# Optimization experiments

Measured on AMD Instinct MI355X. Metric: run time of the kernel, lower is better.

Reference implementation:

```python
import jax, jax.numpy as jnp
import numpy as np

N_NODES = 50000
N_EDGES = 1600000
N_GRAPHS = 64
IN_DIM = 128
HID = 128
N_CLASSES = 10


def setup_inputs() -> dict:
    key = jax.random.key(0)
    ks = jax.random.split(key, 12)
    x = jax.random.normal(ks[0], (N_NODES, IN_DIM), dtype=jnp.float32)
    edge_index = jax.random.randint(ks[1], (2, N_EDGES), 0, N_NODES, dtype=jnp.int32)
    batch = jnp.sort(jax.random.randint(ks[2], (N_NODES,), 0, N_GRAPHS, dtype=jnp.int32))
    def glorot(k, shape):
        s = 1.0 / np.sqrt(shape[0])
        return jax.random.uniform(k, shape, jnp.float32, -s, s)
    W1 = glorot(ks[3], (IN_DIM, HID)); b1 = jnp.zeros((HID,), jnp.float32)
    W2 = glorot(ks[4], (HID, HID));    b2 = jnp.zeros((HID,), jnp.float32)
    Wc1 = glorot(ks[5], (HID, HID));   bc1 = glorot(ks[6], (HID,))
    Wc2 = glorot(ks[7], (HID, N_CLASSES)); bc2 = glorot(ks[8], (N_CLASSES,))
    return {"x": x, "edge_index": edge_index, "batch": batch,
            "W1": W1, "b1": b1, "W2": W2, "b2": b2,
            "Wc1": Wc1, "bc1": bc1, "Wc2": Wc2, "bc2": bc2}


def gcn_conv(x, edge_index, W, b):
    """PyG GCNConv: sym-normalized A-hat (with self loops) @ (x W) + b."""
    n = x.shape[0]
    loop = jnp.arange(n, dtype=edge_index.dtype)
    src = jnp.concatenate([edge_index[0], loop])  # message source
    dst = jnp.concatenate([edge_index[1], loop])  # message target
    deg = jax.ops.segment_sum(jnp.ones_like(src, dtype=x.dtype), dst, num_segments=n)
    dinv = jnp.where(deg > 0, jax.lax.rsqrt(deg), jnp.zeros_like(deg))
    norm = dinv[src] * dinv[dst]  # [E+N]
    h = x @ W                     # [N, H]
    msg = h[src] * norm[:, None]  # gather + scale
    out = jax.ops.segment_sum(msg, dst, num_segments=n)
    return out + b


def reference(x, edge_index, batch, W1, b1, W2, b2, Wc1, bc1, Wc2, bc2):
    h = jax.nn.relu(gcn_conv(x, edge_index, W1, b1))
    h = jax.nn.relu(gcn_conv(h, edge_index, W2, b2))
    # per-graph mean pooling (segment mean)
    sums = jax.ops.segment_sum(h, batch, num_segments=N_GRAPHS)
    cnt = jax.ops.segment_sum(jnp.ones((h.shape[0],), h.dtype), batch, num_segments=N_GRAPHS)
    g = sums / jnp.clip(cnt, 1.0)[:, None]  # [G, H]
    z = jax.nn.relu(g @ Wc1 + bc1)
    return z @ Wc2 + bc2
```

## Files before the change

kernel.cpp:

```cpp
#include <hip/hip_runtime.h>
#include <cstdint>
#include <cstddef>

#define CHUNK 4096

typedef __attribute__((ext_vector_type(8))) short short8;
typedef __attribute__((ext_vector_type(4))) float f32x4;
typedef __attribute__((ext_vector_type(4))) unsigned int u32x4;

__device__ __forceinline__ float bf2f(unsigned short u) {
  return __uint_as_float(((unsigned)u) << 16);
}
__device__ __forceinline__ unsigned short f2bf(float f) {
  unsigned u = __float_as_uint(f);
  u += 0x7fffu + ((u >> 16) & 1u);
  return (unsigned short)(u >> 16);
}

union SMem {
  unsigned short ws[128 * 136];
  struct { int c[256]; int cur[256]; int sb[256]; } cf;
};

__global__ void prep_k(const float* __restrict__ W1, const float* __restrict__ W2,
                       unsigned short* __restrict__ W1t, unsigned short* __restrict__ W2t,
                       int* __restrict__ gcur, int B) {
  int idx = blockIdx.x * 256 + threadIdx.x;
  const float* W = (idx < 16384) ? W1 : W2;
  unsigned short* Wt = (idx < 16384) ? W1t : W2t;
  int i = idx & 16383;
  int k = i >> 7, n = i & 127;
  Wt[n * 128 + k] = f2bf(W[i]);
  if (blockIdx.x == 0 && threadIdx.x < B) gcur[threadIdx.x] = 0;
}

__global__ __launch_bounds__(256) void scatter_atomic_k(const int* __restrict__ src,
                                                        const int* __restrict__ dst, int E,
                                                        int* __restrict__ gcur,
                                                        unsigned int* __restrict__ tmp,
                                                        int cap, int B) {
  __shared__ unsigned pk[CHUNK];
  __shared__ unsigned char bk[CHUNK];
  __shared__ int h[256];
  __shared__ int cur[256];
  __shared__ int base_s[256];
  int t = threadIdx.x;
  h[t] = 0;
  __syncthreads();
  int e0 = blockIdx.x * CHUNK;
  int e1 = e0 + CHUNK; if (e1 > E) e1 = E;
  int m = e1 - e0;
  for (int i = t; i < m; i += 256) {
    int d = dst[e0 + i], s = src[e0 + i];
    int b = d >> 8;
    pk[i] = ((unsigned)s << 8) | (unsigned)(d & 255);
    bk[i] = (unsigned char)b;
    atomicAdd(&h[b], 1);
  }
  __syncthreads();
  if (t < B && h[t] > 0) base_s[t] = atomicAdd(&gcur[t], h[t]);
  cur[t] = 0;
  __syncthreads();
  for (int i = t; i < m; i += 256) {
    int b = bk[i];
    int r = atomicAdd(&cur[b], 1);
    int p = base_s[b] + r;
    if (p < cap) tmp[(size_t)b * cap + p] = pk[i];
  }
}

template <bool AF32>
__device__ __forceinline__ void gemm_tile(SMem& sm, const void* Ap,
                                          const unsigned short* Wt,
                                          unsigned short* C, int N, int tile) {
  for (int idx = threadIdx.x; idx < 2048; idx += 256) {
    int n = idx >> 4, c = idx & 15;
    *(uint4*)&sm.ws[n * 136 + c * 8] = ((const uint4*)Wt)[idx];
  }
  __syncthreads();
  const int w = threadIdx.x >> 6;
  const int lane = threadIdx.x & 63;
  const int quad = lane >> 4, l16 = lane & 15;
  const int rb = tile * 128 + w * 32;
  f32x4 acc[2][8] = {};
  #pragma unroll
  for (int ks = 0; ks < 4; ks++) {
    short8 aF[2];
    #pragma unroll
    for (int m = 0; m < 2; m++) {
      int r = rb + m * 16 + l16;
      short8 a = {};
      if (r < N) {
        if (AF32) {
          const float* ar = (const float*)Ap + (size_t)r * 128 + ks * 32 + quad * 8;
          float4 u0 = *(const float4*)ar;
          float4 u1 = *(const float4*)(ar + 4);
          a[0] = (short)f2bf(u0.x); a[1] = (short)f2bf(u0.y);
          a[2] = (short)f2bf(u0.z); a[3] = (short)f2bf(u0.w);
          a[4] = (short)f2bf(u1.x); a[5] = (short)f2bf(u1.y);
          a[6] = (short)f2bf(u1.z); a[7] = (short)f2bf(u1.w);
        } else {
          a = *(const short8*)((const unsigned short*)Ap + (size_t)r * 128 + ks * 32 + quad * 8);
        }
      }
      aF[m] = a;
    }
    #pragma unroll
    for (int t = 0; t < 8; t++) {
      short8 bF = *(const short8*)&sm.ws[(t * 16 + l16) * 136 + ks * 32 + quad * 8];
      acc[0][t] = __builtin_amdgcn_mfma_f32_16x16x32_bf16(aF[0], bF, acc[0][t], 0, 0, 0);
      acc[1][t] = __builtin_amdgcn_mfma_f32_16x16x32_bf16(aF[1], bF, acc[1][t], 0, 0, 0);
    }
  }
  __syncthreads();
  unsigned short* Cs = sm.ws;
  #pragma unroll
  for (int m = 0; m < 2; m++) {
    int rloc = w * 32 + m * 16 + quad * 4;
    #pragma unroll
    for (int t = 0; t < 8; t++)
      #pragma unroll
      for (int rg = 0; rg < 4; rg++)
        Cs[(rloc + rg) * 132 + t * 16 + l16] = f2bf(acc[m][t][rg]);
  }
  __syncthreads();
  const int r0 = tile * 128;
  for (int idx = threadIdx.x; idx < 2048; idx += 256) {
    int row = idx >> 4, c = idx & 15;
    int rr = r0 + row;
    if (rr < N) {
      uint2 a = *(uint2*)&Cs[row * 132 + c * 8];
      uint2 b = *(uint2*)&Cs[row * 132 + c * 8 + 4];
      ((uint4*)C)[(size_t)rr * 16 + c] = make_uint4(a.x, a.y, b.x, b.y);
    }
  }
}

__global__ __launch_bounds__(256) void cntfill_gemm1_k(const unsigned int* __restrict__ tmp,
                                                       const int* __restrict__ gcur,
                                                       int N, int E, int cap, int B,
                                                       float* __restrict__ dinv,
                                                       int* __restrict__ rs,
                                                       unsigned short* __restrict__ col,
                                                       const float* __restrict__ x,
                                                       const unsigned short* __restrict__ W1t,
                                                       unsigned short* __restrict__ B2) {
  __shared__ SMem sm;
  const int t = threadIdx.x;
  if ((int)blockIdx.x >= B) {
    gemm_tile<true>(sm, x, W1t, B2, N, blockIdx.x - B);
    return;
  }
  int b = blockIdx.x;
  int cb = 0;
  if (t < B) { cb = gcur[t]; if (cb > cap) cb = cap; }
  sm.cf.sb[t] = cb;
  __syncthreads();
  for (int off = 1; off < 256; off <<= 1) {
    int u = (t >= off) ? sm.cf.sb[t - off] : 0;
    __syncthreads();
    sm.cf.sb[t] += u;
    __syncthreads();
  }
  int base_b = (b > 0) ? sm.cf.sb[b - 1] : 0;
  int cnt_b = sm.cf.sb[b] - base_b;
  if (b == 0 && t == 0) rs[N] = sm.cf.sb[B - 1];
  const unsigned* tb = tmp + (size_t)b * cap;
  sm.cf.c[t] = 0;
  __syncthreads();
  for (int i = t; i < cnt_b; i += 256) atomicAdd(&sm.cf.c[tb[i] & 255u], 1);
  __syncthreads();
  int v = sm.cf.c[t];
  sm.cf.cur[t] = v;
  __syncthreads();
  for (int off = 1; off < 256; off <<= 1) {
    int u = (t >= off) ? sm.cf.cur[t - off] : 0;
    __syncthreads();
    sm.cf.cur[t] += u;
    __syncthreads();
  }
  int rsv = base_b + sm.cf.cur[t] - v;
  int node = (b << 8) + t;
  if (node < N) {
    rs[node] = rsv;
    dinv[node] = rsqrtf((float)v + 1.0f);
  }
  __syncthreads();
  sm.cf.cur[t] = rsv;
  __syncthreads();
  for (int i = t; i < cnt_b; i += 256) {
    unsigned u = tb[i];
    int pos = atomicAdd(&sm.cf.cur[u & 255u], 1);
    col[pos] = (unsigned short)(u >> 8);
  }
}

template <bool AF32>
__global__ __launch_bounds__(256) void gemm_bf_k(const void* __restrict__ Ap,
                                                 const unsigned short* __restrict__ Wt,
                                                 unsigned short* __restrict__ C, int N) {
  __shared__ SMem sm;
  gemm_tile<AF32>(sm, Ap, Wt, C, N, blockIdx.x);
}

template <typename CT>
__global__ __launch_bounds__(256) void agg16_k(const unsigned short* __restrict__ h,
                                               const int* __restrict__ rs,
                                               const CT* __restrict__ col,
                                               const float* __restrict__ dinv,
                                               const float* __restrict__ bias,
                                               unsigned short* __restrict__ outp, int n) {
  int wid = (blockIdx.x * blockDim.x + threadIdx.x) >> 6;
  int lane = threadIdx.x & 63;
  if (wid >= n) return;
  const int g = lane >> 4;
  const int l = lane & 15;
  float di = dinv[wid];
  float acc[8];
  {
    uint4 sv = ((const uint4*)(h + (size_t)wid * 128))[l];
    float ws = (g == 0) ? di : 0.f;
    acc[0] = bf2f((unsigned short)sv.x) * ws;
    acc[1] = bf2f((unsigned short)(sv.x >> 16)) * ws;
    acc[2] = bf2f((unsigned short)sv.y) * ws;
    acc[3] = bf2f((unsigned short)(sv.y >> 16)) * ws;
    acc[4] = bf2f((unsigned short)sv.z) * ws;
    acc[5] = bf2f((unsigned short)(sv.z >> 16)) * ws;
    acc[6] = bf2f((unsigned short)sv.w) * ws;
    acc[7] = bf2f((unsigned short)(sv.w >> 16)) * ws;
  }
  int beg = rs[wid], end = rs[wid + 1];
  for (int base = beg; base < end; base += 16) {
    int e0 = base + g, e1 = base + 4 + g, e2 = base + 8 + g, e3 = base + 12 + g;
    int i0 = (e0 < end) ? e0 : end - 1;
    int i1 = (e1 < end) ? e1 : end - 1;
    int i2 = (e2 < end) ? e2 : end - 1;
    int i3 = (e3 < end) ? e3 : end - 1;
    int s0 = (int)col[i0], s1 = (int)col[i1], s2 = (int)col[i2], s3 = (int)col[i3];
    float w0 = (e0 < end) ? dinv[s0] : 0.f;
    float w1 = (e1 < end) ? dinv[s1] : 0.f;
    float w2 = (e2 < end) ? dinv[s2] : 0.f;
    float w3 = (e3 < end) ? dinv[s3] : 0.f;
    uint4 h0 = ((const uint4*)(h + (size_t)s0 * 128))[l];
    uint4 h1 = ((const uint4*)(h + (size_t)s1 * 128))[l];
    uint4 h2 = ((const uint4*)(h + (size_t)s2 * 128))[l];
    uint4 h3 = ((const uint4*)(h + (size_t)s3 * 128))[l];
    acc[0] += bf2f((unsigned short)h0.x) * w0 + bf2f((unsigned short)h1.x) * w1
            + bf2f((unsigned short)h2.x) * w2 + bf2f((unsigned short)h3.x) * w3;
    acc[1] += bf2f((unsigned short)(h0.x >> 16)) * w0 + bf2f((unsigned short)(h1.x >> 16)) * w1
            + bf2f((unsigned short)(h2.x >> 16)) * w2 + bf2f((unsigned short)(h3.x >> 16)) * w3;
    acc[2] += bf2f((unsigned short)h0.y) * w0 + bf2f((unsigned short)h1.y) * w1
            + bf2f((unsigned short)h2.y) * w2 + bf2f((unsigned short)h3.y) * w3;
    acc[3] += bf2f((unsigned short)(h0.y >> 16)) * w0 + bf2f((unsigned short)(h1.y >> 16)) * w1
            + bf2f((unsigned short)(h2.y >> 16)) * w2 + bf2f((unsigned short)(h3.y >> 16)) * w3;
    acc[4] += bf2f((unsigned short)h0.z) * w0 + bf2f((unsigned short)h1.z) * w1
            + bf2f((unsigned short)h2.z) * w2 + bf2f((unsigned short)h3.z) * w3;
    acc[5] += bf2f((unsigned short)(h0.z >> 16)) * w0 + bf2f((unsigned short)(h1.z >> 16)) * w1
            + bf2f((unsigned short)(h2.z >> 16)) * w2 + bf2f((unsigned short)(h3.z >> 16)) * w3;
    acc[6] += bf2f((unsigned short)h0.w) * w0 + bf2f((unsigned short)h1.w) * w1
            + bf2f((unsigned short)h2.w) * w2 + bf2f((unsigned short)h3.w) * w3;
    acc[7] += bf2f((unsigned short)(h0.w >> 16)) * w0 + bf2f((unsigned short)(h1.w >> 16)) * w1
            + bf2f((unsigned short)(h2.w >> 16)) * w2 + bf2f((unsigned short)(h3.w >> 16)) * w3;
  }
  #pragma unroll
  for (int j = 0; j < 8; j++) {
    acc[j] += __shfl_xor(acc[j], 16);
    acc[j] += __shfl_xor(acc[j], 32);
  }
  if (g == 0) {
    float4 bA = *(const float4*)(bias + l * 8);
    float4 bB = *(const float4*)(bias + l * 8 + 4);
    float r0 = fmaxf(acc[0] * di + bA.x, 0.f);
    float r1 = fmaxf(acc[1] * di + bA.y, 0.f);
    float r2 = fmaxf(acc[2] * di + bA.z, 0.f);
    float r3 = fmaxf(acc[3] * di + bA.w, 0.f);
    float r4 = fmaxf(acc[4] * di + bB.x, 0.f);
    float r5 = fmaxf(acc[5] * di + bB.y, 0.f);
    float r6 = fmaxf(acc[6] * di + bB.z, 0.f);
    float r7 = fmaxf(acc[7] * di + bB.w, 0.f);
    u32x4 v;
    v.x = (unsigned)f2bf(r0) | ((unsigned)f2bf(r1) << 16);
    v.y = (unsigned)f2bf(r2) | ((unsigned)f2bf(r3) << 16);
    v.z = (unsigned)f2bf(r4) | ((unsigned)f2bf(r5) << 16);
    v.w = (unsigned)f2bf(r6) | ((unsigned)f2bf(r7) << 16);
    __builtin_nontemporal_store(v, (u32x4*)outp + (size_t)wid * 16 + l);
  }
}

__global__ __launch_bounds__(256) void poolclassify2_k(const unsigned short* __restrict__ h,
                                                       const int* __restrict__ bat, int n,
                                                       const float* __restrict__ Wc1,
                                                       const float* __restrict__ bc1,
                                                       const float* __restrict__ Wc2,
                                                       const float* __restrict__ bc2,
                                                       float* __restrict__ out, int nc) {
  __shared__ float red[16][136];
  __shared__ float gs[128];
  __shared__ float zs[128];
  const int g = blockIdx.x;
  const int t = threadIdx.x;
  const int slot = t >> 4;
  const int seg = t & 15;
  int lo;
  {
    int l = 0, r = n;
    while (l < r) { int m = (l + r) >> 1; if (bat[m] < g) l = m + 1; else r = m; }
    lo = l;
  }
  int hi;
  {
    int l = lo, r = n;
    while (l < r) { int m = (l + r) >> 1; if (bat[m] < g + 1) l = m + 1; else r = m; }
    hi = l;
  }
  float a0 = 0.f, a1 = 0.f, a2 = 0.f, a3 = 0.f, a4 = 0.f, a5 = 0.f, a6 = 0.f, a7 = 0.f;
  for (int i = lo + slot; i < hi; i += 16) {
    uint4 v = ((const uint4*)(h + (size_t)i * 128))[seg];
    a0 += bf2f((unsigned short)v.x);  a1 += bf2f((unsigned short)(v.x >> 16));
    a2 += bf2f((unsigned short)v.y);  a3 += bf2f((unsigned short)(v.y >> 16));
    a4 += bf2f((unsigned short)v.z);  a5 += bf2f((unsigned short)(v.z >> 16));
    a6 += bf2f((unsigned short)v.w);  a7 += bf2f((unsigned short)(v.w >> 16));
  }
  red[slot][seg * 8 + 0] = a0; red[slot][seg * 8 + 1] = a1;
  red[slot][seg * 8 + 2] = a2; red[slot][seg * 8 + 3] = a3;
  red[slot][seg * 8 + 4] = a4; red[slot][seg * 8 + 5] = a5;
  red[slot][seg * 8 + 6] = a6; red[slot][seg * 8 + 7] = a7;
  __syncthreads();
  if (t < 128) {
    float c = (float)(hi - lo); if (c < 1.f) c = 1.f;
    float s = 0.f;
    #pragma unroll
    for (int k = 0; k < 16; k++) s += red[k][t];
    gs[t] = s / c;
  }
  __syncthreads();
  if (t < 128) {
    float a = bc1[t];
    for (int k = 0; k < 128; k++) a += gs[k] * Wc1[k * 128 + t];
    zs[t] = fmaxf(a, 0.f);
  }
  __syncthreads();
  if (t < nc) {
    float o = bc2[t];
    for (int k = 0; k < 128; k++) o += zs[k] * Wc2[k * nc + t];
    out[g * nc + t] = o;
  }
}

__global__ void count_edges_k(const int* __restrict__ dst, int E, int* __restrict__ cnt) {
  int e = blockIdx.x * blockDim.x + threadIdx.x;
  if (e < E) atomicAdd(&cnt[dst[e]], 1);
}
__global__ void dinv_k(const int* __restrict__ cnt, float* __restrict__ dinv, int n) {
  int i = blockIdx.x * blockDim.x + threadIdx.x;
  if (i < n) dinv[i] = rsqrtf((float)cnt[i] + 1.0f);
}
__global__ void fill_csr_k(const int* __restrict__ src, const int* __restrict__ dst, int E,
                           int* __restrict__ cursor, int* __restrict__ col) {
  int e = blockIdx.x * blockDim.x + threadIdx.x;
  if (e < E) {
    int d = dst[e], s = src[e];
    int pos = atomicAdd(&cursor[d], 1);
    col[pos] = s;
  }
}
__global__ void scan1_k(const int* __restrict__ cnt, int* __restrict__ rs,
                        int* __restrict__ partials, int n) {
  __shared__ int s[1024];
  int t = threadIdx.x;
  int gid = blockIdx.x * 1024 + t;
  int v = (gid < n) ? cnt[gid] : 0;
  s[t] = v;
  __syncthreads();
  for (int off = 1; off < 1024; off <<= 1) {
    int u = (t >= off) ? s[t - off] : 0;
    __syncthreads();
    s[t] += u;
    __syncthreads();
  }
  if (gid < n) rs[gid] = s[t] - v;
  if (t == 1023) partials[blockIdx.x] = s[1023];
}
__global__ void scan2_k(int* __restrict__ partials, int nb) {
  if (threadIdx.x == 0 && blockIdx.x == 0) {
    int acc = 0;
    for (int i = 0; i < nb; i++) { int v = partials[i]; partials[i] = acc; acc += v; }
  }
}
__global__ void scan3_k(int* __restrict__ rs, int* __restrict__ cursor,
                        const int* __restrict__ partials, int n, int total) {
  int gid = blockIdx.x * blockDim.x + threadIdx.x;
  if (gid < n) {
    int v = rs[gid] + partials[gid >> 10];
    rs[gid] = v;
    cursor[gid] = v;
  }
  if (gid == 0) rs[n] = total;
}

extern "C" void kernel_launch(void* const* d_in, const int* in_sizes, int n_in,
                              void* d_out, int out_size, void* d_ws, size_t ws_size,
                              hipStream_t stream) {
  const float* x   = (const float*)d_in[0];
  const int*   ei  = (const int*)d_in[1];
  const int*   bat = (const int*)d_in[2];
  const float* W1  = (const float*)d_in[3];
  const float* b1  = (const float*)d_in[4];
  const float* W2  = (const float*)d_in[5];
  const float* b2  = (const float*)d_in[6];
  const float* Wc1 = (const float*)d_in[7];
  const float* bc1 = (const float*)d_in[8];
  const float* Wc2 = (const float*)d_in[9];
  const float* bc2 = (const float*)d_in[10];
  float* out = (float*)d_out;

  const int N  = in_sizes[0] / 128;
  const int E  = in_sizes[1] / 2;
  const int NC = in_sizes[10];
  const int G  = out_size / NC;
  const int* src = ei;
  const int* dst = ei + E;
  (void)n_in; (void)ws_size;

  size_t off = 0;
  auto walloc = [&](size_t bytes) -> void* {
    void* p = (char*)d_ws + off;
    off += (bytes + 255) & ~(size_t)255;
    return p;
  };
  unsigned short* B2 = (unsigned short*)walloc((size_t)N * 128 * 2);
  unsigned short* B3 = (unsigned short*)walloc((size_t)N * 128 * 2);
  unsigned short* W1t = (unsigned short*)walloc(128 * 128 * 2);
  unsigned short* W2t = (unsigned short*)walloc(128 * 128 * 2);
  float* dinv = (float*)walloc((size_t)N * 4);
  int*   rs   = (int*)  walloc((size_t)(N + 1) * 4);

  const bool small = (N <= 65535);
  const int gblocks = (N + 127) / 128;
  const int aggGrid = (N + 3) / 4;

  if (small) {
    const int B    = (N + 255) >> 8;
    const int nblk = (E + CHUNK - 1) / CHUNK;
    const int cap  = (E + B - 1) / B + 2048;
    unsigned short* col = (unsigned short*)walloc((size_t)E * 2);
    unsigned int*   tmp = (unsigned int*)  walloc((size_t)B * cap * 4);
    int* gcur = (int*)walloc((size_t)B * 4);

    prep_k<<<128, 256, 0, stream>>>(W1, W2, W1t, W2t, gcur, B);
    scatter_atomic_k<<<nblk, 256, 0, stream>>>(src, dst, E, gcur, tmp, cap, B);
    cntfill_gemm1_k<<<B + gblocks, 256, 0, stream>>>(tmp, gcur, N, E, cap, B,
                                                     dinv, rs, col, x, W1t, B2);
    agg16_k<unsigned short><<<aggGrid, 256, 0, stream>>>(B2, rs, col, dinv, b1, B3, N);
    gemm_bf_k<false><<<gblocks, 256, 0, stream>>>(B3, W2t, B2, N);
    agg16_k<unsigned short><<<aggGrid, 256, 0, stream>>>(B2, rs, col, dinv, b2, B3, N);
    poolclassify2_k<<<G, 256, 0, stream>>>(B3, bat, N, Wc1, bc1, Wc2, bc2, out, NC);
  } else {
    const int nb = (N + 1023) / 1024;
    int* cnt    = (int*)walloc((size_t)N * 4);
    int* cursor = (int*)walloc((size_t)N * 4);
    int* col    = (int*)walloc((size_t)E * 4);
    int* partials = (int*)walloc(256 * 4);
    prep_k<<<128, 256, 0, stream>>>(W1, W2, W1t, W2t, cnt , 0);
    (void)hipMemsetAsync(cnt, 0, (size_t)N * 4, stream);
    count_edges_k<<<(E + 255) / 256, 256, 0, stream>>>(dst, E, cnt);
    scan1_k<<<nb, 1024, 0, stream>>>(cnt, rs, partials, N);
    scan2_k<<<1, 64, 0, stream>>>(partials, nb);
    scan3_k<<<(N + 255) / 256, 256, 0, stream>>>(rs, cursor, partials, N, E);
    dinv_k<<<(N + 255) / 256, 256, 0, stream>>>(cnt, dinv, N);
    fill_csr_k<<<(E + 255) / 256, 256, 0, stream>>>(src, dst, E, cursor, col);

    gemm_bf_k<true><<<gblocks, 256, 0, stream>>>(x, W1t, B2, N);
    agg16_k<int><<<aggGrid, 256, 0, stream>>>(B2, rs, col, dinv, b1, B3, N);
    gemm_bf_k<false><<<gblocks, 256, 0, stream>>>(B3, W2t, B2, N);
    agg16_k<int><<<aggGrid, 256, 0, stream>>>(B2, rs, col, dinv, b2, B3, N);
    poolclassify2_k<<<G, 256, 0, stream>>>(B3, bat, N, Wc1, bc1, Wc2, bc2, out, NC);
  }
}
```

Baseline: 292.0 us.

## Halve GEMM tile rows and use packed FMA in aggregation kernel

After: 291.6 us. Within noise of the previous version (-0.1%).

```diff
diff --git a/kernel.cpp b/kernel.cpp
--- a/kernel.cpp
+++ b/kernel.cpp
@@ -6,6 +6,7 @@
 
 typedef __attribute__((ext_vector_type(8))) short short8;
 typedef __attribute__((ext_vector_type(4))) float f32x4;
+typedef __attribute__((ext_vector_type(2))) float f32x2;
 typedef __attribute__((ext_vector_type(4))) unsigned int u32x4;
 
 __device__ __forceinline__ float bf2f(unsigned short u) {
@@ -15,6 +16,15 @@
   unsigned u = __float_as_uint(f);
   u += 0x7fffu + ((u >> 16) & 1u);
   return (unsigned short)(u >> 16);
+}
+__device__ __forceinline__ f32x2 unpk(unsigned u) {
+  f32x2 r;
+  r.x = __uint_as_float(u << 16);
+  r.y = __uint_as_float(u & 0xffff0000u);
+  return r;
+}
+__device__ __forceinline__ void pkfma(f32x2& a, f32x2 b, f32x2 c) {
+  asm("v_pk_fma_f32 %0, %1, %2, %0" : "+v"(a) : "v"(b), "v"(c));
 }
 
 union SMem {
@@ -81,51 +91,43 @@
   const int w = threadIdx.x >> 6;
   const int lane = threadIdx.x & 63;
   const int quad = lane >> 4, l16 = lane & 15;
-  const int rb = tile * 128 + w * 32;
-  f32x4 acc[2][8] = {};
+  const int r = tile * 64 + w * 16 + l16;
+  f32x4 acc[8] = {};
   #pragma unroll
   for (int ks = 0; ks < 4; ks++) {
-    short8 aF[2];
-    #pragma unroll
-    for (int m = 0; m < 2; m++) {
-      int r = rb + m * 16 + l16;
-      short8 a = {};
-      if (r < N) {
-        if (AF32) {
-          const float* ar = (const float*)Ap + (size_t)r * 128 + ks * 32 + quad * 8;
-          float4 u0 = *(const float4*)ar;
-          float4 u1 = *(const float4*)(ar + 4);
-          a[0] = (short)f2bf(u0.x); a[1] = (short)f2bf(u0.y);
-          a[2] = (short)f2bf(u0.z); a[3] = (short)f2bf(u0.w);
-          a[4] = (short)f2bf(u1.x); a[5] = (short)f2bf(u1.y);
-          a[6] = (short)f2bf(u1.z); a[7] = (short)f2bf(u1.w);
-        } else {
-          a = *(const short8*)((const unsigned short*)Ap + (size_t)r * 128 + ks * 32 + quad * 8);
-        }
+    short8 a = {};
+    if (r < N) {
+      if (AF32) {
+        const float* ar = (const float*)Ap + (size_t)r * 128 + ks * 32 + quad * 8;
+        float4 u0 = *(const float4*)ar;
+        float4 u1 = *(const float4*)(ar + 4);
+        a[0] = (short)f2bf(u0.x); a[1] = (short)f2bf(u0.y);
+        a[2] = (short)f2bf(u0.z); a[3] = (short)f2bf(u0.w);
+        a[4] = (short)f2bf(u1.x); a[5] = (short)f2bf(u1.y);
+        a[6] = (short)f2bf(u1.z); a[7] = (short)f2bf(u1.w);
+      } else {
+        a = *(const short8*)((const unsigned short*)Ap + (size_t)r * 128 + ks * 32 + quad * 8);
       }
-      aF[m] = a;
     }
     #pragma unroll
     for (int t = 0; t < 8; t++) {
       short8 bF = *(const short8*)&sm.ws[(t * 16 + l16) * 136 + ks * 32 + quad * 8];
-      acc[0][t] = __builtin_amdgcn_mfma_f32_16x16x32_bf16(aF[0], bF, acc[0][t], 0, 0, 0);
-      acc[1][t] = __builtin_amdgcn_mfma_f32_16x16x32_bf16(aF[1], bF, acc[1][t], 0, 0, 0);
+      acc[t] = __builtin_amdgcn_mfma_f32_16x16x32_bf16(a, bF, acc[t], 0, 0, 0);
     }
   }
   __syncthreads();
   unsigned short* Cs = sm.ws;
-  #pragma unroll
-  for (int m = 0; m < 2; m++) {
-    int rloc = w * 32 + m * 16 + quad * 4;
+  {
+    int rloc = w * 16 + quad * 4;
     #pragma unroll
     for (int t = 0; t < 8; t++)
       #pragma unroll
       for (int rg = 0; rg < 4; rg++)
-        Cs[(rloc + rg) * 132 + t * 16 + l16] = f2bf(acc[m][t][rg]);
-  }
-  __syncthreads();
-  const int r0 = tile * 128;
-  for (int idx = threadIdx.x; idx < 2048; idx += 256) {
+        Cs[(rloc + rg) * 132 + t * 16 + l16] = f2bf(acc[t][rg]);
+  }
+  __syncthreads();
+  const int r0 = tile * 64;
+  for (int idx = threadIdx.x; idx < 1024; idx += 256) {
     int row = idx >> 4, c = idx & 15;
     int rr = r0 + row;
     if (rr < N) {
@@ -216,18 +218,15 @@
   const int g = lane >> 4;
   const int l = lane & 15;
   float di = dinv[wid];
-  float acc[8];
+  f32x2 acc2[4];
   {
     uint4 sv = ((const uint4*)(h + (size_t)wid * 128))[l];
     float ws = (g == 0) ? di : 0.f;
-    acc[0] = bf2f((unsigned short)sv.x) * ws;
-    acc[1] = bf2f((unsigned short)(sv.x >> 16)) * ws;
-    acc[2] = bf2f((unsigned short)sv.y) * ws;
-    acc[3] = bf2f((unsigned short)(sv.y >> 16)) * ws;
-    acc[4] = bf2f((unsigned short)sv.z) * ws;
-    acc[5] = bf2f((unsigned short)(sv.z >> 16)) * ws;
-    acc[6] = bf2f((unsigned short)sv.w) * ws;
-    acc[7] = bf2f((unsigned short)(sv.w >> 16)) * ws;
+    f32x2 wv; wv.x = ws; wv.y = ws;
+    acc2[0] = unpk(sv.x) * wv;
+    acc2[1] = unpk(sv.y) * wv;
+    acc2[2] = unpk(sv.z) * wv;
+    acc2[3] = unpk(sv.w) * wv;
   }
   int beg = rs[wid], end = rs[wid + 1];
   for (int base = beg; base < end; base += 16) {
@@ -245,39 +244,37 @@
     uint4 h1 = ((const uint4*)(h + (size_t)s1 * 128))[l];
     uint4 h2 = ((const uint4*)(h + (size_t)s2 * 128))[l];
     uint4 h3 = ((const uint4*)(h + (size_t)s3 * 128))[l];
-    acc[0] += bf2f((unsigned short)h0.x) * w0 + bf2f((unsigned short)h1.x) * w1
-            + bf2f((unsigned short)h2.x) * w2 + bf2f((unsigned short)h3.x) * w3;
-    acc[1] += bf2f((unsigned short)(h0.x >> 16)) * w0 + bf2f((unsigned short)(h1.x >> 16)) * w1
-            + bf2f((unsigned short)(h2.x >> 16)) * w2 + bf2f((unsigned short)(h3.x >> 16)) * w3;
-    acc[2] += bf2f((unsigned short)h0.y) * w0 + bf2f((unsigned short)h1.y) * w1
-            + bf2f((unsigned short)h2.y) * w2 + bf2f((unsigned short)h3.y) * w3;
-    acc[3] += bf2f((unsigned short)(h0.y >> 16)) * w0 + bf2f((unsigned short)(h1.y >> 16)) * w1
-            + bf2f((unsigned short)(h2.y >> 16)) * w2 + bf2f((unsigned short)(h3.y >> 16)) * w3;
-    acc[4] += bf2f((unsigned short)h0.z) * w0 + bf2f((unsigned short)h1.z) * w1
-            + bf2f((unsigned short)h2.z) * w2 + bf2f((unsigned short)h3.z) * w3;
-    acc[5] += bf2f((unsigned short)(h0.z >> 16)) * w0 + bf2f((unsigned short)(h1.z >> 16)) * w1
-            + bf2f((unsigned short)(h2.z >> 16)) * w2 + bf2f((unsigned short)(h3.z >> 16)) * w3;
-    acc[6] += bf2f((unsigned short)h0.w) * w0 + bf2f((unsigned short)h1.w) * w1
-            + bf2f((unsigned short)h2.w) * w2 + bf2f((unsigned short)h3.w) * w3;
-    acc[7] += bf2f((unsigned short)(h0.w >> 16)) * w0 + bf2f((unsigned short)(h1.w >> 16)) * w1
-            + bf2f((unsigned short)(h2.w >> 16)) * w2 + bf2f((unsigned short)(h3.w >> 16)) * w3;
+    f32x2 w0v; w0v.x = w0; w0v.y = w0;
+    f32x2 w1v; w1v.x = w1; w1v.y = w1;
+    f32x2 w2v; w2v.x = w2; w2v.y = w2;
+    f32x2 w3v; w3v.x = w3; w3v.y = w3;
+    pkfma(acc2[0], unpk(h0.x), w0v); pkfma(acc2[0], unpk(h1.x), w1v);
+    pkfma(acc2[0], unpk(h2.x), w2v); pkfma(acc2[0], unpk(h3.x), w3v);
+    pkfma(acc2[1], unpk(h0.y), w0v); pkfma(acc2[1], unpk(h1.y), w1v);
+    pkfma(acc2[1], unpk(h2.y), w2v); pkfma(acc2[1], unpk(h3.y), w3v);
+    pkfma(acc2[2], unpk(h0.z), w0v); pkfma(acc2[2], unpk(h1.z), w1v);
+    pkfma(acc2[2], unpk(h2.z), w2v); pkfma(acc2[2], unpk(h3.z), w3v);
+    pkfma(acc2[3], unpk(h0.w), w0v); pkfma(acc2[3], unpk(h1.w), w1v);
+    pkfma(acc2[3], unpk(h2.w), w2v); pkfma(acc2[3], unpk(h3.w), w3v);
   }
   #pragma unroll
-  for (int j = 0; j < 8; j++) {
-    acc[j] += __shfl_xor(acc[j], 16);
-    acc[j] += __shfl_xor(acc[j], 32);
+  for (int j = 0; j < 4; j++) {
+    acc2[j].x += __shfl_xor(acc2[j].x, 16);
+    acc2[j].y += __shfl_xor(acc2[j].y, 16);
+    acc2[j].x += __shfl_xor(acc2[j].x, 32);
+    acc2[j].y += __shfl_xor(acc2[j].y, 32);
   }
   if (g == 0) {
     float4 bA = *(const float4*)(bias + l * 8);
     float4 bB = *(const float4*)(bias + l * 8 + 4);
-    float r0 = fmaxf(acc[0] * di + bA.x, 0.f);
-    float r1 = fmaxf(acc[1] * di + bA.y, 0.f);
-    float r2 = fmaxf(acc[2] * di + bA.z, 0.f);
-    float r3 = fmaxf(acc[3] * di + bA.w, 0.f);
-    float r4 = fmaxf(acc[4] * di + bB.x, 0.f);
-    float r5 = fmaxf(acc[5] * di + bB.y, 0.f);
-    float r6 = fmaxf(acc[6] * di + bB.z, 0.f);
-    float r7 = fmaxf(acc[7] * di + bB.w, 0.f);
+    float r0 = fmaxf(acc2[0].x * di + bA.x, 0.f);
+    float r1 = fmaxf(acc2[0].y * di + bA.y, 0.f);
+    float r2 = fmaxf(acc2[1].x * di + bA.z, 0.f);
+    float r3 = fmaxf(acc2[1].y * di + bA.w, 0.f);
+    float r4 = fmaxf(acc2[2].x * di + bB.x, 0.f);
+    float r5 = fmaxf(acc2[2].y * di + bB.y, 0.f);
+    float r6 = fmaxf(acc2[3].x * di + bB.z, 0.f);
+    float r7 = fmaxf(acc2[3].y * di + bB.w, 0.f);
     u32x4 v;
     v.x = (unsigned)f2bf(r0) | ((unsigned)f2bf(r1) << 16);
     v.y = (unsigned)f2bf(r2) | ((unsigned)f2bf(r3) << 16);
@@ -436,7 +433,7 @@
   int*   rs   = (int*)  walloc((size_t)(N + 1) * 4);
 
   const bool small = (N <= 65535);
-  const int gblocks = (N + 127) / 128;
+  const int gblocks = (N + 63) / 64;
   const int aggGrid = (N + 3) / 4;
 
   if (small) {
```
